# Kernel optimization log

Hardware: AMD Instinct MI355X
Metric: run time of the kernel (lower is better)

Reference implementation:

```python
import jax, jax.numpy as jnp
import numpy as np

N_NODES = 50000
N_EDGES = 800000
C = 128
EDGE_DIM = 8
N_LAYERS = 3


def setup_inputs() -> dict:
    key = jax.random.key(0)
    ks = jax.random.split(key, 8)
    x = jax.random.normal(ks[0], (N_NODES, C), dtype=jnp.float32)
    edge_index = jax.random.randint(ks[1], (2, N_EDGES), 0, N_NODES, dtype=jnp.int64)
    edge_attr = jax.random.uniform(ks[2], (N_EDGES, EDGE_DIM), dtype=jnp.float32)
    # stacked per-layer params (all layers are 128->128 HydroConv)
    lin_w = jax.random.normal(ks[3], (N_LAYERS, C, C), dtype=jnp.float32) / np.sqrt(C)
    lin_b = jnp.zeros((N_LAYERS, C), dtype=jnp.float32)
    emlp_w = jax.random.normal(ks[4], (N_LAYERS, EDGE_DIM, 1), dtype=jnp.float32) / np.sqrt(EDGE_DIM)
    emlp_b = jnp.zeros((N_LAYERS, 1), dtype=jnp.float32)
    return {"x": x, "edge_index": edge_index, "edge_attr": edge_attr,
            "lin_w": lin_w, "lin_b": lin_b, "emlp_w": emlp_w, "emlp_b": emlp_b}


def _hydro_conv(x, src, dst, edge_attr, lw, lb, ew, eb):
    # edge weight: softplus(edge_attr @ ew + eb) -> [E, 1]
    weight = jax.nn.softplus(edge_attr @ ew + eb)
    # message: weight * (x_j - x_i), x_j = source, x_i = target
    msg = weight * (x[src] - x[dst])                  # [E, C]
    agg = jax.ops.segment_sum(msg, dst, num_segments=N_NODES)  # scatter-add at target
    return agg @ lw + lb                              # node linear


def reference(x, edge_index, edge_attr, lin_w, lin_b, emlp_w, emlp_b):
    src, dst = edge_index[0], edge_index[1]
    for i in range(N_LAYERS):
        residual = x
        x = _hydro_conv(x, src, dst, edge_attr, lin_w[i], lin_b[i], emlp_w[i], emlp_b[i])
        if i < N_LAYERS - 1:
            x = jax.nn.relu(x)
            x = x + residual  # residual=True, dropout=0
    return x
```

## Files before the change

kernel.cpp:

```cpp
#include <hip/hip_runtime.h>

#define NN 50000
#define NE 800000
#define CC 128
#define NL 3

typedef short bf16x8 __attribute__((ext_vector_type(8)));
typedef float f32x4 __attribute__((ext_vector_type(4)));
union U16 { uint4 u; bf16x8 v; };

__device__ __forceinline__ float b2f(unsigned short u) {
  return __uint_as_float(((unsigned int)u) << 16);
}
__device__ __forceinline__ unsigned short f2b(float f) {
  unsigned int x = __float_as_uint(f);
  x += 0x7fffu + ((x >> 16) & 1u);
  return (unsigned short)(x >> 16);
}

__global__ void k_flags(const unsigned short* __restrict__ x,
                        const int* __restrict__ ei, int* __restrict__ flags) {
  __shared__ int cnt, any;
  if (threadIdx.x == 0) { cnt = 0; any = 0; }
  __syncthreads();
  if (threadIdx.x < 128) {
    unsigned short u = x[2 * threadIdx.x];
    int ex = (u >> 7) & 0xFF;
    if (ex >= 0x70 && ex <= 0x8F) atomicAdd(&cnt, 1);
  }
  if (ei[2 * threadIdx.x + 1] != 0) atomicOr(&any, 1);
  __syncthreads();
  if (threadIdx.x == 0) {
    flags[0] = (cnt >= 64) ? 1 : 0;
    flags[1] = (any == 0) ? 1 : 0;
  }
}

__device__ __forceinline__ int eidx(const int* ei, int row, int e, int f64) {
  return f64 ? ei[2 * ((size_t)row * NE + e)] : ei[(size_t)row * NE + e];
}

__global__ __launch_bounds__(256) void k_cvt_x(const void* __restrict__ xin,
                                               unsigned short* __restrict__ xb,
                                               const int* __restrict__ flags) {
  if (flags[0]) return;
  int i = blockIdx.x * 256 + threadIdx.x;
  const float4 a = ((const float4*)xin)[2 * i];
  const float4 b = ((const float4*)xin)[2 * i + 1];
  uint4 o;
  o.x = (unsigned)f2b(a.x) | ((unsigned)f2b(a.y) << 16);
  o.y = (unsigned)f2b(a.z) | ((unsigned)f2b(a.w) << 16);
  o.z = (unsigned)f2b(b.x) | ((unsigned)f2b(b.y) << 16);
  o.w = (unsigned)f2b(b.z) | ((unsigned)f2b(b.w) << 16);
  ((uint4*)xb)[i] = o;
}

__global__ __launch_bounds__(256) void k_cvt_par(const void* lw, const void* lb,
                                                 const void* emw, const void* emb,
                                                 unsigned short* __restrict__ wt,
                                                 float* lbf, float* emwf, float* embf,
                                                 const int* __restrict__ flags) {
  int i = blockIdx.x * 256 + threadIdx.x;
  const int bf = flags[0];
  if (i < NL * CC * CC) {
    unsigned short v = bf ? ((const unsigned short*)lw)[i]
                          : f2b(((const float*)lw)[i]);
    const int l = i >> 14, r = i & 16383, k = r >> 7, n = r & 127;
    wt[l * 16384 + n * 128 + k] = v;
  }
  if (i < NL * CC)
    lbf[i] = bf ? b2f(((const unsigned short*)lb)[i]) : ((const float*)lb)[i];
  if (i < NL * 8)
    emwf[i] = bf ? b2f(((const unsigned short*)emw)[i]) : ((const float*)emw)[i];
  if (i < NL)
    embf[i] = bf ? b2f(((const unsigned short*)emb)[i]) : ((const float*)emb)[i];
}

#define HT 8
#define HIST_BLKS ((NE + HT * 256 - 1) / (HT * 256))
__global__ __launch_bounds__(256) void k_hist(const int* __restrict__ ei,
                                              int* __restrict__ deg,
                                              unsigned short* __restrict__ rank,
                                              const int* __restrict__ flags) {
  const int f64 = flags[1];
  const int nt = gridDim.x * 256;
  const int t = blockIdx.x * 256 + threadIdx.x;
  int d[HT], r[HT];
#pragma unroll
  for (int k = 0; k < HT; ++k) {
    const int e = t + k * nt;
    d[k] = (e < NE) ? eidx(ei, 1, e, f64) : -1;
  }
#pragma unroll
  for (int k = 0; k < HT; ++k)
    if (d[k] >= 0) r[k] = atomicAdd(&deg[d[k]], 1);
#pragma unroll
  for (int k = 0; k < HT; ++k) {
    const int e = t + k * nt;
    if (e < NE) rank[e] = (unsigned short)r[k];
  }
}

#define NI4 (NN / 4)
#define SCAN_BLKS ((NI4 + 255) / 256)
__global__ __launch_bounds__(256) void k_scan1(const int* __restrict__ deg,
                                               int* __restrict__ offs,
                                               int* __restrict__ bsum) {
  __shared__ int ls[256];
  const int t = threadIdx.x;
  const int g = blockIdx.x * 256 + t;
  int4 d = make_int4(0, 0, 0, 0);
  if (g < NI4) d = ((const int4*)deg)[g];
  const int s = d.x + d.y + d.z + d.w;
  ls[t] = s;
  __syncthreads();
#pragma unroll
  for (int off = 1; off < 256; off <<= 1) {
    int tmp = (t >= off) ? ls[t - off] : 0;
    __syncthreads();
    ls[t] += tmp;
    __syncthreads();
  }
  const int excl = ls[t] - s;
  if (g < NI4) {
    int4 o;
    o.x = excl; o.y = o.x + d.x; o.z = o.y + d.y; o.w = o.z + d.z;
    ((int4*)offs)[g] = o;
  }
  if (t == 255) bsum[blockIdx.x] = ls[255];
}

__global__ void k_scan2(const int* __restrict__ bsum, int* __restrict__ bbase,
                        int* __restrict__ offs) {
  if (threadIdx.x == 0) {
    int run = 0;
    for (int b = 0; b < SCAN_BLKS; ++b) { bbase[b] = run; run += bsum[b]; }
    offs[NN] = run;
  }
}

__global__ __launch_bounds__(256) void k_scan3(int* __restrict__ offs,
                                               const int* __restrict__ bbase) {
  const int g = blockIdx.x * 256 + threadIdx.x;
  if (g >= NI4) return;
  const int base = bbase[blockIdx.x];
  int4 o = ((int4*)offs)[g];
  o.x += base; o.y += base; o.z += base; o.w += base;
  ((int4*)offs)[g] = o;
}

__global__ __launch_bounds__(256) void k_fill(const int* __restrict__ ei,
                                              const void* __restrict__ ea,
                                              const float* __restrict__ emwf,
                                              const float* __restrict__ embf,
                                              const int* __restrict__ offs,
                                              const unsigned short* __restrict__ rank,
                                              uint4* __restrict__ esrt,
                                              const int* __restrict__ flags) {
  int e = blockIdx.x * 256 + threadIdx.x;
  if (e >= NE) return;
  float a[8];
  if (flags[0]) {
    const uint4 v = ((const uint4*)ea)[e];
    unsigned int p[4] = {v.x, v.y, v.z, v.w};
#pragma unroll
    for (int q = 0; q < 4; ++q) {
      a[2 * q]     = __uint_as_float(p[q] << 16);
      a[2 * q + 1] = __uint_as_float(p[q] & 0xffff0000u);
    }
  } else {
    const float4 v0 = ((const float4*)ea)[2 * e];
    const float4 v1 = ((const float4*)ea)[2 * e + 1];
    a[0] = v0.x; a[1] = v0.y; a[2] = v0.z; a[3] = v0.w;
    a[4] = v1.x; a[5] = v1.y; a[6] = v1.z; a[7] = v1.w;
  }
  float w[NL];
#pragma unroll
  for (int l = 0; l < NL; ++l) {
    float z = embf[l];
#pragma unroll
    for (int k = 0; k < 8; ++k) z += a[k] * emwf[l * 8 + k];
    w[l] = (z > 20.f) ? z : log1pf(expf(z));
  }
  const int f64 = flags[1];
  const int d = eidx(ei, 1, e, f64);
  const int s = eidx(ei, 0, e, f64);
  const int pos = offs[d] + (int)rank[e];
  esrt[pos] = make_uint4((unsigned)s, __float_as_uint(w[0]),
                         __float_as_uint(w[1]), __float_as_uint(w[2]));
}

template<int LAYER>
__device__ __forceinline__ float wsel(const uint4& p) {
  return __uint_as_float(LAYER == 0 ? p.y : (LAYER == 1 ? p.z : p.w));
}

template<int LAYER>
__global__ __launch_bounds__(256) void k_gather(const int* __restrict__ offs,
                                                const uint4* __restrict__ esrt,
                                                const unsigned short* xb_,
                                                const unsigned short* alt,
                                                int sel,
                                                unsigned short* __restrict__ agg,
                                                const int* __restrict__ flags) {
  const unsigned short* xb = (sel && flags[0]) ? alt : xb_;
  const int node =
      __builtin_amdgcn_readfirstlane(blockIdx.x * 4 + (threadIdx.x >> 6));
  const int c = (threadIdx.x & 63) * 2;
  float ax = 0.f, ay = 0.f, sw = 0.f;
  int j = offs[node];
  const int j1 = offs[node + 1];
  for (; j + 8 <= j1; j += 8) {
    const uint4 p0 = esrt[j],     p1 = esrt[j + 1], p2 = esrt[j + 2], p3 = esrt[j + 3];
    const uint4 p4 = esrt[j + 4], p5 = esrt[j + 5], p6 = esrt[j + 6], p7 = esrt[j + 7];
    const unsigned v0 = *(const unsigned*)&xb[(size_t)p0.x * CC + c];
    const unsigned v1 = *(const unsigned*)&xb[(size_t)p1.x * CC + c];
    const unsigned v2 = *(const unsigned*)&xb[(size_t)p2.x * CC + c];
    const unsigned v3 = *(const unsigned*)&xb[(size_t)p3.x * CC + c];
    const unsigned v4 = *(const unsigned*)&xb[(size_t)p4.x * CC + c];
    const unsigned v5 = *(const unsigned*)&xb[(size_t)p5.x * CC + c];
    const unsigned v6 = *(const unsigned*)&xb[(size_t)p6.x * CC + c];
    const unsigned v7 = *(const unsigned*)&xb[(size_t)p7.x * CC + c];
    const float w0 = wsel<LAYER>(p0), w1 = wsel<LAYER>(p1);
    const float w2 = wsel<LAYER>(p2), w3 = wsel<LAYER>(p3);
    const float w4 = wsel<LAYER>(p4), w5 = wsel<LAYER>(p5);
    const float w6 = wsel<LAYER>(p6), w7 = wsel<LAYER>(p7);
    ax += w0 * __uint_as_float(v0 << 16) + w1 * __uint_as_float(v1 << 16)
        + w2 * __uint_as_float(v2 << 16) + w3 * __uint_as_float(v3 << 16)
        + w4 * __uint_as_float(v4 << 16) + w5 * __uint_as_float(v5 << 16)
        + w6 * __uint_as_float(v6 << 16) + w7 * __uint_as_float(v7 << 16);
    ay += w0 * __uint_as_float(v0 & 0xffff0000u) + w1 * __uint_as_float(v1 & 0xffff0000u)
        + w2 * __uint_as_float(v2 & 0xffff0000u) + w3 * __uint_as_float(v3 & 0xffff0000u)
        + w4 * __uint_as_float(v4 & 0xffff0000u) + w5 * __uint_as_float(v5 & 0xffff0000u)
        + w6 * __uint_as_float(v6 & 0xffff0000u) + w7 * __uint_as_float(v7 & 0xffff0000u);
    sw += w0 + w1 + w2 + w3 + w4 + w5 + w6 + w7;
  }
  for (; j + 4 <= j1; j += 4) {
    const uint4 p0 = esrt[j], p1 = esrt[j + 1], p2 = esrt[j + 2], p3 = esrt[j + 3];
    const float w0 = wsel<LAYER>(p0), w1 = wsel<LAYER>(p1);
    const float w2 = wsel<LAYER>(p2), w3 = wsel<LAYER>(p3);
    const unsigned v0 = *(const unsigned*)&xb[(size_t)p0.x * CC + c];
    const unsigned v1 = *(const unsigned*)&xb[(size_t)p1.x * CC + c];
    const unsigned v2 = *(const unsigned*)&xb[(size_t)p2.x * CC + c];
    const unsigned v3 = *(const unsigned*)&xb[(size_t)p3.x * CC + c];
    ax += w0 * __uint_as_float(v0 << 16) + w1 * __uint_as_float(v1 << 16)
        + w2 * __uint_as_float(v2 << 16) + w3 * __uint_as_float(v3 << 16);
    ay += w0 * __uint_as_float(v0 & 0xffff0000u) + w1 * __uint_as_float(v1 & 0xffff0000u)
        + w2 * __uint_as_float(v2 & 0xffff0000u) + w3 * __uint_as_float(v3 & 0xffff0000u);
    sw += w0 + w1 + w2 + w3;
  }
  for (; j < j1; ++j) {
    const uint4 p0 = esrt[j];
    const float w0 = wsel<LAYER>(p0);
    const unsigned v0 = *(const unsigned*)&xb[(size_t)p0.x * CC + c];
    ax += w0 * __uint_as_float(v0 << 16);
    ay += w0 * __uint_as_float(v0 & 0xffff0000u);
    sw += w0;
  }
  const unsigned xi = *(const unsigned*)&xb[(size_t)node * CC + c];
  const float rx = ax - sw * __uint_as_float(xi << 16);
  const float ry = ay - sw * __uint_as_float(xi & 0xffff0000u);
  *(unsigned*)&agg[(size_t)node * CC + c] =
      (unsigned)f2b(rx) | ((unsigned)f2b(ry) << 16);
}

#define LPAD 136
__global__ __launch_bounds__(256) void k_gemm(unsigned short* agg,
                                              const unsigned short* xc_,
                                              const unsigned short* alt,
                                              int sel,
                                              const unsigned short* __restrict__ wt,
                                              const float* __restrict__ lbf,
                                              int layer, void* outp, int last,
                                              const int* __restrict__ flags) {
  const unsigned short* xc = (sel && flags[0]) ? alt : xc_;
  __shared__ unsigned short shA[64 * LPAD];
  __shared__ unsigned short shB[128 * LPAD];
  const int rb = blockIdx.x * 64;
  const unsigned short* wtl = wt + (size_t)layer * CC * CC;

  for (int u = threadIdx.x; u < 1024; u += 256) {
    const int row = u >> 4, q = u & 15;
    uint4 v = make_uint4(0, 0, 0, 0);
    if (rb + row < NN) v = *(const uint4*)&agg[(size_t)(rb + row) * CC + q * 8];
    *(uint4*)&shA[row * LPAD + q * 8] = v;
  }
  for (int u = threadIdx.x; u < 2048; u += 256) {
    const int row = u >> 4, q = u & 15;
    *(uint4*)&shB[row * LPAD + q * 8] = *(const uint4*)&wtl[row * 128 + q * 8];
  }
  __syncthreads();

  const int w = threadIdx.x >> 6;
  const int l = threadIdx.x & 63;
  const int lr = l & 15;
  const int lk = (l >> 4) * 8;

  U16 afr[4];
#pragma unroll
  for (int kk = 0; kk < 4; ++kk)
    afr[kk].u = *(const uint4*)&shA[(w * 16 + lr) * LPAD + kk * 32 + lk];

  const float* lbp = lbf + layer * CC;
  f32x4 acc[8];
#pragma unroll
  for (int t = 0; t < 8; ++t) {
    acc[t] = (f32x4){0.f, 0.f, 0.f, 0.f};
#pragma unroll
    for (int kk = 0; kk < 4; ++kk) {
      U16 bfr;
      bfr.u = *(const uint4*)&shB[(t * 16 + lr) * LPAD + kk * 32 + lk];
      acc[t] = __builtin_amdgcn_mfma_f32_16x16x32_bf16(afr[kk].v, bfr.v, acc[t], 0, 0, 0);
    }
  }

#pragma unroll
  for (int t = 0; t < 8; ++t) {
    const float bv = lbp[t * 16 + lr];
#pragma unroll
    for (int r = 0; r < 4; ++r) {
      const int tr = (l >> 4) * 4 + r;
      shA[(w * 16 + tr) * LPAD + t * 16 + lr] = f2b(acc[t][r] + bv);
    }
  }
  const int isbf = flags[0];
#pragma unroll
  for (int i = 0; i < 8; ++i) {
    const int idx = i * 64 + l;
    const int row = idx >> 5, cg = idx & 31;
    const int gr = rb + w * 16 + row;
    if (gr >= NN) continue;
    const uint2 yv = *(const uint2*)&shA[(w * 16 + row) * LPAD + cg * 4];
    float y0 = __uint_as_float(yv.x << 16);
    float y1 = __uint_as_float(yv.x & 0xffff0000u);
    float y2 = __uint_as_float(yv.y << 16);
    float y3 = __uint_as_float(yv.y & 0xffff0000u);
    const size_t off = (size_t)gr * CC + cg * 4;
    if (!last) {
      const uint2 rv = *(const uint2*)&xc[off];
      y0 = fmaxf(y0, 0.f) + __uint_as_float(rv.x << 16);
      y1 = fmaxf(y1, 0.f) + __uint_as_float(rv.x & 0xffff0000u);
      y2 = fmaxf(y2, 0.f) + __uint_as_float(rv.y << 16);
      y3 = fmaxf(y3, 0.f) + __uint_as_float(rv.y & 0xffff0000u);
      *(uint2*)&agg[off] = make_uint2((unsigned)f2b(y0) | ((unsigned)f2b(y1) << 16),
                                      (unsigned)f2b(y2) | ((unsigned)f2b(y3) << 16));
    } else if (isbf) {
      *(uint2*)&((unsigned short*)outp)[off] = yv;
    } else {
      *(float4*)&((float*)outp)[off] = make_float4(y0, y1, y2, y3);
    }
  }
}

extern "C" void kernel_launch(void* const* d_in, const int* in_sizes, int n_in,
                              void* d_out, int out_size, void* d_ws, size_t ws_size,
                              hipStream_t stream) {
  const unsigned short* x0 = (const unsigned short*)d_in[0];
  const int* ei = (const int*)d_in[1];

  const size_t nbuf = (size_t)NN * CC;
  unsigned short* xb0 = (unsigned short*)d_ws;
  unsigned short* xb1 = xb0 + nbuf;
  unsigned short* wt = xb1 + nbuf;
  uint4* esrt = (uint4*)(wt + (size_t)NL * CC * CC);
  int* deg = (int*)(esrt + NE);
  int* offs = deg + NN;
  unsigned short* rank = (unsigned short*)(offs + NN + 4);
  int* bsum = (int*)(rank + NE);
  int* bbase = bsum + 64;
  float* lbf = (float*)(bbase + 64);
  float* emwf = lbf + (size_t)NL * CC;
  float* embf = emwf + NL * 8;
  int* flags = (int*)(embf + NL);
  const size_t need = (size_t)((char*)(flags + 2) - (char*)d_ws);
  if (ws_size < need) {
    hipMemsetAsync(d_out, 0, (size_t)out_size * 2, stream);
    return;
  }

  k_flags<<<1, 256, 0, stream>>>(x0, ei, flags);
  k_cvt_x<<<(NN * CC / 8) / 256, 256, 0, stream>>>(d_in[0], xb0, flags);
  k_cvt_par<<<(NL * CC * CC + 255) / 256, 256, 0, stream>>>(
      d_in[3], d_in[4], d_in[5], d_in[6], wt, lbf, emwf, embf, flags);

  hipMemsetAsync(deg, 0, NN * sizeof(int), stream);
  k_hist<<<HIST_BLKS, 256, 0, stream>>>(ei, deg, rank, flags);
  k_scan1<<<SCAN_BLKS, 256, 0, stream>>>(deg, offs, bsum);
  k_scan2<<<1, 64, 0, stream>>>(bsum, bbase, offs);
  k_scan3<<<SCAN_BLKS, 256, 0, stream>>>(offs, bbase);
  k_fill<<<(NE + 255) / 256, 256, 0, stream>>>(ei, d_in[2], emwf, embf,
                                               offs, rank, esrt, flags);

  unsigned short* xc = xb0;
  unsigned short* ag = xb1;
  for (int layer = 0; layer < NL; ++layer) {
    const int sel = (layer == 0) ? 1 : 0;
    if (layer == 0)
      k_gather<0><<<NN / 4, 256, 0, stream>>>(offs, esrt, xc, x0, sel, ag, flags);
    else if (layer == 1)
      k_gather<1><<<NN / 4, 256, 0, stream>>>(offs, esrt, xc, x0, sel, ag, flags);
    else
      k_gather<2><<<NN / 4, 256, 0, stream>>>(offs, esrt, xc, x0, sel, ag, flags);
    k_gemm<<<(NN + 63) / 64, 256, 0, stream>>>(ag, xc, x0, sel, wt, lbf, layer,
                                               d_out, layer == NL - 1 ? 1 : 0, flags);
    unsigned short* t = xc; xc = ag; ag = t;
  }
}
```

Measured before the change: 317.7 us.

## Switch gather to edge-balanced segments with fp32 atomic accumulation

The gather kernel now gives each wavefront a fixed chunk of 32 destination-sorted edges instead of one node. It keeps a running sum per destination and flushes partial sums with fp32 atomicAdd into a float aggregation buffer. The GEMM converts that buffer to bf16 on load, zeroes it for the next layer, and writes the new activations to a separate output buffer. This balances work across nodes with uneven degree, but adds atomics, a 25.6MB fp32 buffer with extra read, write and zeroing traffic, and packs src and dst into 16 bits each, which cannot hold node ids above 65535.

```diff
diff --git a/kernel.cpp b/kernel.cpp
--- a/kernel.cpp
+++ b/kernel.cpp
@@ -186,93 +186,93 @@
   const int d = eidx(ei, 1, e, f64);
   const int s = eidx(ei, 0, e, f64);
   const int pos = offs[d] + (int)rank[e];
-  esrt[pos] = make_uint4((unsigned)s, __float_as_uint(w[0]),
-                         __float_as_uint(w[1]), __float_as_uint(w[2]));
-}
-
+  esrt[pos] = make_uint4((unsigned)s | ((unsigned)d << 16),
+                         __float_as_uint(w[0]), __float_as_uint(w[1]),
+                         __float_as_uint(w[2]));
+}
+
+#define EPW 32
+#define GB (EPW / 8)
 template<int LAYER>
-__device__ __forceinline__ float wsel(const uint4& p) {
-  return __uint_as_float(LAYER == 0 ? p.y : (LAYER == 1 ? p.z : p.w));
+__device__ __forceinline__ unsigned wcomp(const uint4& p) {
+  return LAYER == 0 ? p.y : (LAYER == 1 ? p.z : p.w);
 }
 
 template<int LAYER>
-__global__ __launch_bounds__(256) void k_gather(const int* __restrict__ offs,
-                                                const uint4* __restrict__ esrt,
+__global__ __launch_bounds__(256) void k_gather(const uint4* __restrict__ esrt,
                                                 const unsigned short* xb_,
-                                                const unsigned short* alt,
-                                                int sel,
-                                                unsigned short* __restrict__ agg,
+                                                const unsigned short* alt, int sel,
+                                                float* __restrict__ aggf,
                                                 const int* __restrict__ flags) {
   const unsigned short* xb = (sel && flags[0]) ? alt : xb_;
-  const int node =
-      __builtin_amdgcn_readfirstlane(blockIdx.x * 4 + (threadIdx.x >> 6));
+  const int wv = blockIdx.x * 4 + (threadIdx.x >> 6);
+  int e = wv * EPW;
   const int c = (threadIdx.x & 63) * 2;
   float ax = 0.f, ay = 0.f, sw = 0.f;
-  int j = offs[node];
-  const int j1 = offs[node + 1];
-  for (; j + 8 <= j1; j += 8) {
-    const uint4 p0 = esrt[j],     p1 = esrt[j + 1], p2 = esrt[j + 2], p3 = esrt[j + 3];
-    const uint4 p4 = esrt[j + 4], p5 = esrt[j + 5], p6 = esrt[j + 6], p7 = esrt[j + 7];
-    const unsigned v0 = *(const unsigned*)&xb[(size_t)p0.x * CC + c];
-    const unsigned v1 = *(const unsigned*)&xb[(size_t)p1.x * CC + c];
-    const unsigned v2 = *(const unsigned*)&xb[(size_t)p2.x * CC + c];
-    const unsigned v3 = *(const unsigned*)&xb[(size_t)p3.x * CC + c];
-    const unsigned v4 = *(const unsigned*)&xb[(size_t)p4.x * CC + c];
-    const unsigned v5 = *(const unsigned*)&xb[(size_t)p5.x * CC + c];
-    const unsigned v6 = *(const unsigned*)&xb[(size_t)p6.x * CC + c];
-    const unsigned v7 = *(const unsigned*)&xb[(size_t)p7.x * CC + c];
-    const float w0 = wsel<LAYER>(p0), w1 = wsel<LAYER>(p1);
-    const float w2 = wsel<LAYER>(p2), w3 = wsel<LAYER>(p3);
-    const float w4 = wsel<LAYER>(p4), w5 = wsel<LAYER>(p5);
-    const float w6 = wsel<LAYER>(p6), w7 = wsel<LAYER>(p7);
-    ax += w0 * __uint_as_float(v0 << 16) + w1 * __uint_as_float(v1 << 16)
-        + w2 * __uint_as_float(v2 << 16) + w3 * __uint_as_float(v3 << 16)
-        + w4 * __uint_as_float(v4 << 16) + w5 * __uint_as_float(v5 << 16)
-        + w6 * __uint_as_float(v6 << 16) + w7 * __uint_as_float(v7 << 16);
-    ay += w0 * __uint_as_float(v0 & 0xffff0000u) + w1 * __uint_as_float(v1 & 0xffff0000u)
-        + w2 * __uint_as_float(v2 & 0xffff0000u) + w3 * __uint_as_float(v3 & 0xffff0000u)
-        + w4 * __uint_as_float(v4 & 0xffff0000u) + w5 * __uint_as_float(v5 & 0xffff0000u)
-        + w6 * __uint_as_float(v6 & 0xffff0000u) + w7 * __uint_as_float(v7 & 0xffff0000u);
-    sw += w0 + w1 + w2 + w3 + w4 + w5 + w6 + w7;
-  }
-  for (; j + 4 <= j1; j += 4) {
-    const uint4 p0 = esrt[j], p1 = esrt[j + 1], p2 = esrt[j + 2], p3 = esrt[j + 3];
-    const float w0 = wsel<LAYER>(p0), w1 = wsel<LAYER>(p1);
-    const float w2 = wsel<LAYER>(p2), w3 = wsel<LAYER>(p3);
-    const unsigned v0 = *(const unsigned*)&xb[(size_t)p0.x * CC + c];
-    const unsigned v1 = *(const unsigned*)&xb[(size_t)p1.x * CC + c];
-    const unsigned v2 = *(const unsigned*)&xb[(size_t)p2.x * CC + c];
-    const unsigned v3 = *(const unsigned*)&xb[(size_t)p3.x * CC + c];
-    ax += w0 * __uint_as_float(v0 << 16) + w1 * __uint_as_float(v1 << 16)
-        + w2 * __uint_as_float(v2 << 16) + w3 * __uint_as_float(v3 << 16);
-    ay += w0 * __uint_as_float(v0 & 0xffff0000u) + w1 * __uint_as_float(v1 & 0xffff0000u)
-        + w2 * __uint_as_float(v2 & 0xffff0000u) + w3 * __uint_as_float(v3 & 0xffff0000u);
-    sw += w0 + w1 + w2 + w3;
-  }
-  for (; j < j1; ++j) {
-    const uint4 p0 = esrt[j];
-    const float w0 = wsel<LAYER>(p0);
-    const unsigned v0 = *(const unsigned*)&xb[(size_t)p0.x * CC + c];
-    ax += w0 * __uint_as_float(v0 << 16);
-    ay += w0 * __uint_as_float(v0 & 0xffff0000u);
-    sw += w0;
-  }
-  const unsigned xi = *(const unsigned*)&xb[(size_t)node * CC + c];
-  const float rx = ax - sw * __uint_as_float(xi << 16);
-  const float ry = ay - sw * __uint_as_float(xi & 0xffff0000u);
-  *(unsigned*)&agg[(size_t)node * CC + c] =
-      (unsigned)f2b(rx) | ((unsigned)f2b(ry) << 16);
+  int dcur = -1;
+  unsigned xdv = 0;
+  uint4 P[8], Q[8];
+#pragma unroll
+  for (int k = 0; k < 8; ++k) P[k] = esrt[e + k];
+#pragma unroll
+  for (int b = 0; b < GB; ++b) {
+    unsigned sd[8]; float w8[8];
+#pragma unroll
+    for (int k = 0; k < 8; ++k) {
+      sd[k] = (unsigned)__builtin_amdgcn_readfirstlane((int)P[k].x);
+      w8[k] = __uint_as_float(
+          (unsigned)__builtin_amdgcn_readfirstlane((int)wcomp<LAYER>(P[k])));
+    }
+    unsigned v[8];
+#pragma unroll
+    for (int k = 0; k < 8; ++k) {
+      const unsigned short* row = xb + (size_t)(sd[k] & 0xffffu) * CC;
+      v[k] = *(const unsigned*)&row[c];
+    }
+    if (b + 1 < GB) {
+#pragma unroll
+      for (int k = 0; k < 8; ++k) Q[k] = esrt[e + 8 + k];
+    }
+#pragma unroll
+    for (int k = 0; k < 8; ++k) {
+      const int d = (int)(sd[k] >> 16);
+      if (d != dcur) {
+        if (dcur >= 0) {
+          float* ar = aggf + (size_t)dcur * CC + c;
+          atomicAdd(ar,     ax - sw * __uint_as_float(xdv << 16));
+          atomicAdd(ar + 1, ay - sw * __uint_as_float(xdv & 0xffff0000u));
+        }
+        ax = 0.f; ay = 0.f; sw = 0.f;
+        dcur = d;
+        xdv = *(const unsigned*)&xb[(size_t)d * CC + c];
+      }
+      ax += w8[k] * __uint_as_float(v[k] << 16);
+      ay += w8[k] * __uint_as_float(v[k] & 0xffff0000u);
+      sw += w8[k];
+    }
+    if (b + 1 < GB) {
+#pragma unroll
+      for (int k = 0; k < 8; ++k) P[k] = Q[k];
+    }
+    e += 8;
+  }
+  if (dcur >= 0) {
+    float* ar = aggf + (size_t)dcur * CC + c;
+    atomicAdd(ar,     ax - sw * __uint_as_float(xdv << 16));
+    atomicAdd(ar + 1, ay - sw * __uint_as_float(xdv & 0xffff0000u));
+  }
 }
 
 #define LPAD 136
-__global__ __launch_bounds__(256) void k_gemm(unsigned short* agg,
+__global__ __launch_bounds__(256) void k_gemm(float* __restrict__ aggf,
                                               const unsigned short* xc_,
                                               const unsigned short* alt,
                                               int sel,
                                               const unsigned short* __restrict__ wt,
                                               const float* __restrict__ lbf,
                                               int layer, void* outp, int last,
-                                              const int* __restrict__ flags) {
+                                              const int* __restrict__ flags,
+                                              unsigned short* __restrict__ xout) {
   const unsigned short* xc = (sel && flags[0]) ? alt : xc_;
   __shared__ unsigned short shA[64 * LPAD];
   __shared__ unsigned short shB[128 * LPAD];
@@ -281,15 +281,31 @@
 
   for (int u = threadIdx.x; u < 1024; u += 256) {
     const int row = u >> 4, q = u & 15;
-    uint4 v = make_uint4(0, 0, 0, 0);
-    if (rb + row < NN) v = *(const uint4*)&agg[(size_t)(rb + row) * CC + q * 8];
-    *(uint4*)&shA[row * LPAD + q * 8] = v;
+    uint4 o = make_uint4(0, 0, 0, 0);
+    if (rb + row < NN) {
+      const float4 a = *(const float4*)&aggf[(size_t)(rb + row) * CC + q * 8];
+      const float4 b = *(const float4*)&aggf[(size_t)(rb + row) * CC + q * 8 + 4];
+      o.x = (unsigned)f2b(a.x) | ((unsigned)f2b(a.y) << 16);
+      o.y = (unsigned)f2b(a.z) | ((unsigned)f2b(a.w) << 16);
+      o.z = (unsigned)f2b(b.x) | ((unsigned)f2b(b.y) << 16);
+      o.w = (unsigned)f2b(b.z) | ((unsigned)f2b(b.w) << 16);
+    }
+    *(uint4*)&shA[row * LPAD + q * 8] = o;
   }
   for (int u = threadIdx.x; u < 2048; u += 256) {
     const int row = u >> 4, q = u & 15;
     *(uint4*)&shB[row * LPAD + q * 8] = *(const uint4*)&wtl[row * 128 + q * 8];
   }
   __syncthreads();
+
+  if (!last) {
+    for (int u = threadIdx.x; u < 2048; u += 256) {
+      const int row = u >> 5, q = u & 31;
+      if (rb + row < NN)
+        *(float4*)&aggf[(size_t)(rb + row) * CC + q * 4] =
+            make_float4(0.f, 0.f, 0.f, 0.f);
+    }
+  }
 
   const int w = threadIdx.x >> 6;
   const int l = threadIdx.x & 63;
@@ -342,8 +358,8 @@
       y1 = fmaxf(y1, 0.f) + __uint_as_float(rv.x & 0xffff0000u);
       y2 = fmaxf(y2, 0.f) + __uint_as_float(rv.y << 16);
       y3 = fmaxf(y3, 0.f) + __uint_as_float(rv.y & 0xffff0000u);
-      *(uint2*)&agg[off] = make_uint2((unsigned)f2b(y0) | ((unsigned)f2b(y1) << 16),
-                                      (unsigned)f2b(y2) | ((unsigned)f2b(y3) << 16));
+      *(uint2*)&xout[off] = make_uint2((unsigned)f2b(y0) | ((unsigned)f2b(y1) << 16),
+                                       (unsigned)f2b(y2) | ((unsigned)f2b(y3) << 16));
     } else if (isbf) {
       *(uint2*)&((unsigned short*)outp)[off] = yv;
     } else {
@@ -363,7 +379,8 @@
   unsigned short* xb1 = xb0 + nbuf;
   unsigned short* wt = xb1 + nbuf;
   uint4* esrt = (uint4*)(wt + (size_t)NL * CC * CC);
-  int* deg = (int*)(esrt + NE);
+  float* aggf = (float*)(esrt + NE);
+  int* deg = (int*)(aggf + nbuf);
   int* offs = deg + NN;
   unsigned short* rank = (unsigned short*)(offs + NN + 4);
   int* bsum = (int*)(rank + NE);
@@ -384,6 +401,7 @@
       d_in[3], d_in[4], d_in[5], d_in[6], wt, lbf, emwf, embf, flags);
 
   hipMemsetAsync(deg, 0, NN * sizeof(int), stream);
+  hipMemsetAsync(aggf, 0, nbuf * sizeof(float), stream);
   k_hist<<<HIST_BLKS, 256, 0, stream>>>(ei, deg, rank, flags);
   k_scan1<<<SCAN_BLKS, 256, 0, stream>>>(deg, offs, bsum);
   k_scan2<<<1, 64, 0, stream>>>(bsum, bbase, offs);
@@ -391,18 +409,20 @@
   k_fill<<<(NE + 255) / 256, 256, 0, stream>>>(ei, d_in[2], emwf, embf,
                                                offs, rank, esrt, flags);
 
+  const int GATHER_BLKS = (NE / EPW) / 4;
   unsigned short* xc = xb0;
   unsigned short* ag = xb1;
   for (int layer = 0; layer < NL; ++layer) {
     const int sel = (layer == 0) ? 1 : 0;
     if (layer == 0)
-      k_gather<0><<<NN / 4, 256, 0, stream>>>(offs, esrt, xc, x0, sel, ag, flags);
+      k_gather<0><<<GATHER_BLKS, 256, 0, stream>>>(esrt, xc, x0, sel, aggf, flags);
     else if (layer == 1)
-      k_gather<1><<<NN / 4, 256, 0, stream>>>(offs, esrt, xc, x0, sel, ag, flags);
+      k_gather<1><<<GATHER_BLKS, 256, 0, stream>>>(esrt, xc, x0, sel, aggf, flags);
     else
-      k_gather<2><<<NN / 4, 256, 0, stream>>>(offs, esrt, xc, x0, sel, ag, flags);
-    k_gemm<<<(NN + 63) / 64, 256, 0, stream>>>(ag, xc, x0, sel, wt, lbf, layer,
-                                               d_out, layer == NL - 1 ? 1 : 0, flags);
+      k_gather<2><<<GATHER_BLKS, 256, 0, stream>>>(esrt, xc, x0, sel, aggf, flags);
+    k_gemm<<<(NN + 63) / 64, 256, 0, stream>>>(aggf, xc, x0, sel, wt, lbf, layer,
+                                               d_out, layer == NL - 1 ? 1 : 0,
+                                               flags, ag);
     unsigned short* t = xc; xc = ag; ag = t;
   }
 }
```

After: 434.7 us. 36.8% more time.

## Restructure gather: 16-byte row loads, 4 edges per wave step, shuffle-broadcast records

Applied to the files above, without the earlier changes.

The gather kernel now splits each wave into 4 groups of 16 lanes. Each lane loads 8 bf16 channels with a 16-byte load, so 4 neighbor rows are fetched at once. Edge records are loaded cooperatively, one per lane in chunks of 64, and broadcast with shuffles instead of every lane reading every record. Partial sums are reduced across groups with xor shuffles at the end. This cuts redundant record loads and widens memory transactions, in exchange for shuffle overhead and wasted lanes on low-degree nodes.

```diff
diff --git a/kernel.cpp b/kernel.cpp
--- a/kernel.cpp
+++ b/kernel.cpp
@@ -191,77 +191,95 @@
 }
 
 template<int LAYER>
-__device__ __forceinline__ float wsel(const uint4& p) {
-  return __uint_as_float(LAYER == 0 ? p.y : (LAYER == 1 ? p.z : p.w));
+__device__ __forceinline__ unsigned wcomp(const uint4& p) {
+  return LAYER == 0 ? p.y : (LAYER == 1 ? p.z : p.w);
 }
 
 template<int LAYER>
 __global__ __launch_bounds__(256) void k_gather(const int* __restrict__ offs,
                                                 const uint4* __restrict__ esrt,
                                                 const unsigned short* xb_,
-                                                const unsigned short* alt,
-                                                int sel,
+                                                const unsigned short* alt, int sel,
                                                 unsigned short* __restrict__ agg,
                                                 const int* __restrict__ flags) {
   const unsigned short* xb = (sel && flags[0]) ? alt : xb_;
   const int node =
       __builtin_amdgcn_readfirstlane(blockIdx.x * 4 + (threadIdx.x >> 6));
-  const int c = (threadIdx.x & 63) * 2;
-  float ax = 0.f, ay = 0.f, sw = 0.f;
-  int j = offs[node];
+  const int l = threadIdx.x & 63;
+  const int g = l >> 4;
+  const int ch = (l & 15) * 8;
+  const int j0 = offs[node];
   const int j1 = offs[node + 1];
-  for (; j + 8 <= j1; j += 8) {
-    const uint4 p0 = esrt[j],     p1 = esrt[j + 1], p2 = esrt[j + 2], p3 = esrt[j + 3];
-    const uint4 p4 = esrt[j + 4], p5 = esrt[j + 5], p6 = esrt[j + 6], p7 = esrt[j + 7];
-    const unsigned v0 = *(const unsigned*)&xb[(size_t)p0.x * CC + c];
-    const unsigned v1 = *(const unsigned*)&xb[(size_t)p1.x * CC + c];
-    const unsigned v2 = *(const unsigned*)&xb[(size_t)p2.x * CC + c];
-    const unsigned v3 = *(const unsigned*)&xb[(size_t)p3.x * CC + c];
-    const unsigned v4 = *(const unsigned*)&xb[(size_t)p4.x * CC + c];
-    const unsigned v5 = *(const unsigned*)&xb[(size_t)p5.x * CC + c];
-    const unsigned v6 = *(const unsigned*)&xb[(size_t)p6.x * CC + c];
-    const unsigned v7 = *(const unsigned*)&xb[(size_t)p7.x * CC + c];
-    const float w0 = wsel<LAYER>(p0), w1 = wsel<LAYER>(p1);
-    const float w2 = wsel<LAYER>(p2), w3 = wsel<LAYER>(p3);
-    const float w4 = wsel<LAYER>(p4), w5 = wsel<LAYER>(p5);
-    const float w6 = wsel<LAYER>(p6), w7 = wsel<LAYER>(p7);
-    ax += w0 * __uint_as_float(v0 << 16) + w1 * __uint_as_float(v1 << 16)
-        + w2 * __uint_as_float(v2 << 16) + w3 * __uint_as_float(v3 << 16)
-        + w4 * __uint_as_float(v4 << 16) + w5 * __uint_as_float(v5 << 16)
-        + w6 * __uint_as_float(v6 << 16) + w7 * __uint_as_float(v7 << 16);
-    ay += w0 * __uint_as_float(v0 & 0xffff0000u) + w1 * __uint_as_float(v1 & 0xffff0000u)
-        + w2 * __uint_as_float(v2 & 0xffff0000u) + w3 * __uint_as_float(v3 & 0xffff0000u)
-        + w4 * __uint_as_float(v4 & 0xffff0000u) + w5 * __uint_as_float(v5 & 0xffff0000u)
-        + w6 * __uint_as_float(v6 & 0xffff0000u) + w7 * __uint_as_float(v7 & 0xffff0000u);
-    sw += w0 + w1 + w2 + w3 + w4 + w5 + w6 + w7;
-  }
-  for (; j + 4 <= j1; j += 4) {
-    const uint4 p0 = esrt[j], p1 = esrt[j + 1], p2 = esrt[j + 2], p3 = esrt[j + 3];
-    const float w0 = wsel<LAYER>(p0), w1 = wsel<LAYER>(p1);
-    const float w2 = wsel<LAYER>(p2), w3 = wsel<LAYER>(p3);
-    const unsigned v0 = *(const unsigned*)&xb[(size_t)p0.x * CC + c];
-    const unsigned v1 = *(const unsigned*)&xb[(size_t)p1.x * CC + c];
-    const unsigned v2 = *(const unsigned*)&xb[(size_t)p2.x * CC + c];
-    const unsigned v3 = *(const unsigned*)&xb[(size_t)p3.x * CC + c];
-    ax += w0 * __uint_as_float(v0 << 16) + w1 * __uint_as_float(v1 << 16)
-        + w2 * __uint_as_float(v2 << 16) + w3 * __uint_as_float(v3 << 16);
-    ay += w0 * __uint_as_float(v0 & 0xffff0000u) + w1 * __uint_as_float(v1 & 0xffff0000u)
-        + w2 * __uint_as_float(v2 & 0xffff0000u) + w3 * __uint_as_float(v3 & 0xffff0000u);
-    sw += w0 + w1 + w2 + w3;
-  }
-  for (; j < j1; ++j) {
-    const uint4 p0 = esrt[j];
-    const float w0 = wsel<LAYER>(p0);
-    const unsigned v0 = *(const unsigned*)&xb[(size_t)p0.x * CC + c];
-    ax += w0 * __uint_as_float(v0 << 16);
-    ay += w0 * __uint_as_float(v0 & 0xffff0000u);
-    sw += w0;
-  }
-  const unsigned xi = *(const unsigned*)&xb[(size_t)node * CC + c];
-  const float rx = ax - sw * __uint_as_float(xi << 16);
-  const float ry = ay - sw * __uint_as_float(xi & 0xffff0000u);
-  *(unsigned*)&agg[(size_t)node * CC + c] =
-      (unsigned)f2b(rx) | ((unsigned)f2b(ry) << 16);
+
+  const uint4 xi = *(const uint4*)&xb[(size_t)node * CC + ch];
+
+  float ax[8];
+#pragma unroll
+  for (int i = 0; i < 8; ++i) ax[i] = 0.f;
+  float sw = 0.f;
+
+  for (int jc = j0; jc < j1; jc += 64) {
+    const int cnt = j1 - jc;
+    const int kk = (l < cnt) ? l : (cnt - 1);
+    const uint4 rec = esrt[jc + kk];
+    const int srcl = (int)rec.x;
+    const int wl = (int)wcomp<LAYER>(rec);
+    const int nsb = (cnt + 15) >> 4;
+    for (int b2 = 0; b2 < nsb; ++b2) {
+      int srcw[4]; float wv[4];
+#pragma unroll
+      for (int b = 0; b < 4; ++b) {
+        const int k = b2 * 16 + b * 4 + g;
+        srcw[b] = __shfl(srcl, k);
+        const float w = __uint_as_float((unsigned)__shfl(wl, k));
+        wv[b] = (k < cnt) ? w : 0.f;
+      }
+      uint4 v[4];
+#pragma unroll
+      for (int b = 0; b < 4; ++b)
+        v[b] = *(const uint4*)&xb[(size_t)(unsigned)srcw[b] * CC + ch];
+#pragma unroll
+      for (int b = 0; b < 4; ++b) {
+        const float w = wv[b];
+        const unsigned pv0 = v[b].x, pv1 = v[b].y, pv2 = v[b].z, pv3 = v[b].w;
+        ax[0] += w * __uint_as_float(pv0 << 16);
+        ax[1] += w * __uint_as_float(pv0 & 0xffff0000u);
+        ax[2] += w * __uint_as_float(pv1 << 16);
+        ax[3] += w * __uint_as_float(pv1 & 0xffff0000u);
+        ax[4] += w * __uint_as_float(pv2 << 16);
+        ax[5] += w * __uint_as_float(pv2 & 0xffff0000u);
+        ax[6] += w * __uint_as_float(pv3 << 16);
+        ax[7] += w * __uint_as_float(pv3 & 0xffff0000u);
+        sw += w;
+      }
+    }
+  }
+
+#pragma unroll
+  for (int i = 0; i < 8; ++i) {
+    ax[i] += __shfl_xor(ax[i], 16);
+    ax[i] += __shfl_xor(ax[i], 32);
+  }
+  sw += __shfl_xor(sw, 16);
+  sw += __shfl_xor(sw, 32);
+
+  if (l < 16) {
+    float r[8];
+    r[0] = ax[0] - sw * __uint_as_float(xi.x << 16);
+    r[1] = ax[1] - sw * __uint_as_float(xi.x & 0xffff0000u);
+    r[2] = ax[2] - sw * __uint_as_float(xi.y << 16);
+    r[3] = ax[3] - sw * __uint_as_float(xi.y & 0xffff0000u);
+    r[4] = ax[4] - sw * __uint_as_float(xi.z << 16);
+    r[5] = ax[5] - sw * __uint_as_float(xi.z & 0xffff0000u);
+    r[6] = ax[6] - sw * __uint_as_float(xi.w << 16);
+    r[7] = ax[7] - sw * __uint_as_float(xi.w & 0xffff0000u);
+    uint4 o;
+    o.x = (unsigned)f2b(r[0]) | ((unsigned)f2b(r[1]) << 16);
+    o.y = (unsigned)f2b(r[2]) | ((unsigned)f2b(r[3]) << 16);
+    o.z = (unsigned)f2b(r[4]) | ((unsigned)f2b(r[5]) << 16);
+    o.w = (unsigned)f2b(r[6]) | ((unsigned)f2b(r[7]) << 16);
+    *(uint4*)&agg[(size_t)node * CC + ch] = o;
+  }
 }
 
 #define LPAD 136
```

Result: faster. 308.5 us (-2.9%).
